# Optimization experiments

Hardware: AMD Instinct MI355X
Metric: run time of the kernel (lower is better)

The kernel has to match this reference:

```python
import jax, jax.numpy as jnp
import numpy as np

RADIUS = 3  # local window half-size -> K = (2*RADIUS+1)**2 = 49 taps


def _bilinear_sample_zeros(img_flat, x, y, h, w):
    """Bilinear sampling with zeros padding (grid_sample, align_corners=True).
    img_flat: (B, C, H*W); x, y: (P, K) pixel-space coords. Returns (B, C, P, K).
    align_corners=True denormalization exactly inverts the normalization in the
    original module, so we sample directly at pixel coordinates.
    """
    B, C, _ = img_flat.shape
    x0 = jnp.floor(x)
    y0 = jnp.floor(y)
    out = jnp.zeros((B, C) + x.shape, dtype=img_flat.dtype)
    corners = [
        (x0,       y0,       (x0 + 1 - x) * (y0 + 1 - y)),
        (x0 + 1.0, y0,       (x - x0) * (y0 + 1 - y)),
        (x0,       y0 + 1.0, (x0 + 1 - x) * (y - y0)),
        (x0 + 1.0, y0 + 1.0, (x - x0) * (y - y0)),
    ]
    for xi, yi, wt in corners:
        inb = (xi >= 0) & (xi < w) & (yi >= 0) & (yi < h)
        xi_c = jnp.clip(xi, 0, w - 1).astype(jnp.int32)
        yi_c = jnp.clip(yi, 0, h - 1).astype(jnp.int32)
        idx = (yi_c * w + xi_c).reshape(-1)            # (P*K,)
        v = jnp.take(img_flat, idx, axis=2)            # (B, C, P*K)
        v = v.reshape(B, C, *x.shape)                  # (B, C, P, K)
        out = out + v * (wt * inb.astype(img_flat.dtype))[None, None]
    return out


def reference(feature0, feature1):
    n, c, s, h, w = feature0.shape
    B = n * s
    f0 = feature0.transpose(0, 2, 1, 3, 4).reshape(B, c, h, w)
    f1 = feature1.transpose(0, 2, 1, 3, 4).reshape(B, c, h, w)

    r = RADIUS
    # base pixel coords (x, y), flattened row-major over (h, w) -> (P, 2)
    yy, xx = jnp.meshgrid(jnp.arange(h, dtype=jnp.float32),
                          jnp.arange(w, dtype=jnp.float32), indexing='ij')
    base = jnp.stack([xx, yy], axis=-1).reshape(h * w, 2)  # (P, 2)

    # window offsets (dx, dy), dy outer / dx inner ordering -> (K, 2)
    dys, dxs = jnp.meshgrid(jnp.arange(-r, r + 1, dtype=jnp.float32),
                            jnp.arange(-r, r + 1, dtype=jnp.float32), indexing='ij')
    offs = jnp.stack([dxs, dys], axis=-1).reshape(-1, 2)   # (K, 2)

    sample = base[:, None, :] + offs[None, :, :]           # (P, K, 2)
    valid = ((sample[..., 0] >= 0) & (sample[..., 0] < w) &
             (sample[..., 1] >= 0) & (sample[..., 1] < h))  # (P, K)

    f1_flat = f1.reshape(B, c, h * w)
    wf = _bilinear_sample_zeros(f1_flat, sample[..., 0], sample[..., 1], h, w)  # (B, c, P, K)

    f0_flat = f0.reshape(B, c, h * w)
    corr = jnp.einsum('bcp,bcpk->bpk', f0_flat, wf) / jnp.asarray(c, jnp.float32) ** 0.5
    corr = jnp.where(valid[None], corr, -jnp.inf)
    prob = jax.nn.softmax(corr, axis=-1)                   # (B, P, K)

    corresp = jnp.einsum('bpk,pkj->bpj', prob, sample)     # (B, P, 2) expected (x, y)
    flow = corresp - base[None]                            # (B, P, 2)
    flow = flow.reshape(n, s, h, w, 2).transpose(0, 4, 1, 2, 3)  # (n, 2, s, h, w)
    return flow


def setup_inputs() -> dict:
    key = jax.random.key(0)
    k0, k1 = jax.random.split(key)
    n, c, s, h, w = 2, 64, 4, 64, 44
    feature0 = jax.random.normal(k0, (n, c, s, h, w), dtype=jnp.float32)
    feature1 = jax.random.normal(k1, (n, c, s, h, w), dtype=jnp.float32)
    return {"feature0": feature0, "feature1": feature1}
```

## Files before the change

### kernel.cpp

```cpp
#include <hip/hip_runtime.h>
#include <math.h>

#define N_  2
#define C_  64
#define S_  4
#define H_  64
#define W_  44
#define HW_       (H_ * W_)
#define CH_STRIDE (S_ * HW_)
#define NSTRIDE   (C_ * S_ * HW_)

__global__ __launch_bounds__(448) void flow_kernel(
    const float* __restrict__ f0,
    const float* __restrict__ f1,
    float* __restrict__ out)
{
    const int lane = threadIdx.x & 63;
    const int wid  = threadIdx.x >> 6;

    const int b = blockIdx.x & 7;
    const int y = blockIdx.x >> 3;
    const int n_idx = b >> 2;
    const int s_idx = b & 3;
    const int base  = n_idx * NSTRIDE + s_idx * HW_;

    __shared__ float corr[64][49];

    const int x   = lane;
    const int row = y + wid - 3;
    const bool row_ok = (row >= 0) && (row < H_);

    if (row_ok) {
        const int xc = min(x, W_ - 1);
        const float* f0p = f0 + base + y * W_ + xc;
        const float* f1p = f1 + base + row * W_ + xc;

        float acc[7];
        #pragma unroll
        for (int dx = 0; dx < 7; ++dx) acc[dx] = 0.0f;

        int sidx[7];
        #pragma unroll
        for (int dx = 0; dx < 7; ++dx)
            sidx[dx] = min(max(lane + dx - 3, 0), 63) << 2;

        #pragma unroll 4
        for (int ch = 0; ch < C_; ++ch) {
            const float a = f0p[(size_t)ch * CH_STRIDE];
            const float v = f1p[(size_t)ch * CH_STRIDE];
            #pragma unroll
            for (int dx = 0; dx < 7; ++dx) {
                float t;
                if (dx == 3) {
                    t = v;
                } else {
                    t = __int_as_float(__builtin_amdgcn_ds_bpermute(
                            sidx[dx], __float_as_int(v)));
                }
                acc[dx] = fmaf(a, t, acc[dx]);
            }
        }

        if (x < W_) {
            #pragma unroll
            for (int dx = 0; dx < 7; ++dx) {
                const int col = x + dx - 3;
                const bool ok = (col >= 0) && (col < W_);
                corr[x][wid * 7 + dx] = ok ? acc[dx] * 0.125f : -1e30f;
            }
        }
    } else {
        if (x < W_) {
            #pragma unroll
            for (int dx = 0; dx < 7; ++dx)
                corr[x][wid * 7 + dx] = -1e30f;
        }
    }

    __syncthreads();

    if (wid == 0) {
        float c[49];
        float m = -1e30f;
        #pragma unroll
        for (int k = 0; k < 49; ++k) {
            c[k] = corr[lane][k];
            m = fmaxf(m, c[k]);
        }
        float S = 0.0f, Sx = 0.0f, Sy = 0.0f;
        #pragma unroll
        for (int k = 0; k < 49; ++k) {
            const float e = __expf(c[k] - m);
            S  += e;
            Sx += e * (float)(k % 7 - 3);
            Sy += e * (float)(k / 7 - 3);
        }
        if (lane < W_) {
            const float inv = 1.0f / S;
            const int ob = (n_idx * 2) * S_ * HW_ + s_idx * HW_ + y * W_ + lane;
            out[ob]            = Sx * inv;
            out[ob + S_ * HW_] = Sy * inv;
        }
    }
}

extern "C" void kernel_launch(void* const* d_in, const int* in_sizes, int n_in,
                              void* d_out, int out_size, void* d_ws, size_t ws_size,
                              hipStream_t stream) {
    const float* f0 = (const float*)d_in[0];
    const float* f1 = (const float*)d_in[1];
    float* out = (float*)d_out;

    flow_kernel<<<8 * H_, 448, 0, stream>>>(f0, f1, out);
}
```

Measured before the change: 77.36 us.

## Stage f1 rows in LDS as fp16 and use fdot2 for correlation

Replaces the per-channel cross-lane bpermute shuffles with an LDS slab per wave that holds the f1 row converted to fp16, packed 8 channels per entry and zero-padded at the borders. The dot products then run as packed fdot2 over 8 channels at a time, and the validity masking moves into the softmax stage. The aim is to cut the shuffle traffic and roughly halve the FMA instruction count. The price is fp16 rounding of both features, which may loosen accuracy against the fp32 reference, plus extra LDS use.

```diff
diff --git a/kernel.cpp b/kernel.cpp
--- a/kernel.cpp
+++ b/kernel.cpp
@@ -9,6 +9,19 @@
 #define HW_       (H_ * W_)
 #define CH_STRIDE (S_ * HW_)
 #define NSTRIDE   (C_ * S_ * HW_)
+#define XP  51
+
+typedef _Float16 h2 __attribute__((ext_vector_type(2)));
+typedef _Float16 h8 __attribute__((ext_vector_type(8)));
+
+#if defined(__has_builtin)
+#  if __has_builtin(__builtin_amdgcn_fdot2)
+#    define FDOT2(a, b, c) __builtin_amdgcn_fdot2((a), (b), (c), false)
+#  endif
+#endif
+#ifndef FDOT2
+#  define FDOT2(a, b, c) ((float)(a).x * (float)(b).x + (float)(a).y * (float)(b).y + (c))
+#endif
 
 __global__ __launch_bounds__(448) void flow_kernel(
     const float* __restrict__ f0,
@@ -24,57 +37,75 @@
     const int s_idx = b & 3;
     const int base  = n_idx * NSTRIDE + s_idx * HW_;
 
-    __shared__ float corr[64][49];
+    __shared__ __align__(16) _Float16 ldsf1[7 * 8 * XP * 8];
+    __shared__ float corr[W_][49];
 
     const int x   = lane;
+    const int xe  = min(x, W_ - 1);
     const int row = y + wid - 3;
     const bool row_ok = (row >= 0) && (row < H_);
 
+    float acc[7] = {0.f, 0.f, 0.f, 0.f, 0.f, 0.f, 0.f};
+
     if (row_ok) {
-        const int xc = min(x, W_ - 1);
-        const float* f0p = f0 + base + y * W_ + xc;
-        const float* f1p = f1 + base + row * W_ + xc;
+        const int  xi       = (lane < 44) ? (lane + 3) : ((lane < 47) ? (lane - 44) : lane);
+        const bool do_write = (lane <= 50);
+        const bool real     = (lane < 44);
 
-        float acc[7];
-        #pragma unroll
-        for (int dx = 0; dx < 7; ++dx) acc[dx] = 0.0f;
+        const float* f1p = f1 + base + row * W_ + xe;
+        const float* f0p = f0 + base + y   * W_ + xe;
 
-        int sidx[7];
+        _Float16* slab = ldsf1 + wid * (8 * XP * 8);
+
+        #pragma unroll 2
+        for (int c8 = 0; c8 < 8; ++c8) {
+            const float* cp1 = f1p + (size_t)(c8 * 8) * CH_STRIDE;
+            const float* cp0 = f0p + (size_t)(c8 * 8) * CH_STRIDE;
+
+            float v[8], a[8];
+            #pragma unroll
+            for (int j = 0; j < 8; ++j) v[j] = cp1[(size_t)j * CH_STRIDE];
+            #pragma unroll
+            for (int j = 0; j < 8; ++j) a[j] = cp0[(size_t)j * CH_STRIDE];
+
+            h8 pk;
+            #pragma unroll
+            for (int j = 0; j < 8; ++j)
+                pk[j] = real ? (_Float16)v[j] : (_Float16)0.0f;
+
+            if (do_write)
+                *(h8*)&slab[(c8 * XP + xi) * 8] = pk;
+
+            h2 a2[4];
+            #pragma unroll
+            for (int j = 0; j < 4; ++j) {
+                h2 t; t.x = (_Float16)a[2 * j]; t.y = (_Float16)a[2 * j + 1];
+                a2[j] = t;
+            }
+
+            const _Float16* rp = &slab[(c8 * XP + xe) * 8];
+            #pragma unroll
+            for (int dx = 0; dx < 7; ++dx) {
+                const h8 t = *(const h8*)&rp[dx * 8];
+                h2 t01, t23, t45, t67;
+                t01.x = t[0]; t01.y = t[1];
+                t23.x = t[2]; t23.y = t[3];
+                t45.x = t[4]; t45.y = t[5];
+                t67.x = t[6]; t67.y = t[7];
+                float s = acc[dx];
+                s = FDOT2(a2[0], t01, s);
+                s = FDOT2(a2[1], t23, s);
+                s = FDOT2(a2[2], t45, s);
+                s = FDOT2(a2[3], t67, s);
+                acc[dx] = s;
+            }
+        }
+    }
+
+    if (x < W_) {
         #pragma unroll
         for (int dx = 0; dx < 7; ++dx)
-            sidx[dx] = min(max(lane + dx - 3, 0), 63) << 2;
-
-        #pragma unroll 4
-        for (int ch = 0; ch < C_; ++ch) {
-            const float a = f0p[(size_t)ch * CH_STRIDE];
-            const float v = f1p[(size_t)ch * CH_STRIDE];
-            #pragma unroll
-            for (int dx = 0; dx < 7; ++dx) {
-                float t;
-                if (dx == 3) {
-                    t = v;
-                } else {
-                    t = __int_as_float(__builtin_amdgcn_ds_bpermute(
-                            sidx[dx], __float_as_int(v)));
-                }
-                acc[dx] = fmaf(a, t, acc[dx]);
-            }
-        }
-
-        if (x < W_) {
-            #pragma unroll
-            for (int dx = 0; dx < 7; ++dx) {
-                const int col = x + dx - 3;
-                const bool ok = (col >= 0) && (col < W_);
-                corr[x][wid * 7 + dx] = ok ? acc[dx] * 0.125f : -1e30f;
-            }
-        }
-    } else {
-        if (x < W_) {
-            #pragma unroll
-            for (int dx = 0; dx < 7; ++dx)
-                corr[x][wid * 7 + dx] = -1e30f;
-        }
+            corr[x][wid * 7 + dx] = acc[dx] * 0.125f;
     }
 
     __syncthreads();
@@ -84,8 +115,13 @@
         float m = -1e30f;
         #pragma unroll
         for (int k = 0; k < 49; ++k) {
-            c[k] = corr[lane][k];
-            m = fmaxf(m, c[k]);
+            const int dy  = k / 7, dx = k % 7;
+            const int col = x + dx - 3;
+            const int rr  = y + dy - 3;
+            const bool ok = (col >= 0) && (col < W_) && (rr >= 0) && (rr < H_);
+            const float v = ok ? corr[xe][k] : -1e30f;
+            c[k] = v;
+            m = fmaxf(m, v);
         }
         float S = 0.0f, Sx = 0.0f, Sy = 0.0f;
         #pragma unroll
```

After: 68.32 us. -11.7%, faster.
